# Performance work log

Measured on AMD Instinct MI355X. Metric: run time of the kernel, lower is better.

The kernel has to match this reference:

```python
import jax, jax.numpy as jnp
import numpy as np

N = 100000   # nodes
E = 1250000  # directed edges
K = 20000    # selected nodes
D_IN, D_H, D_OUT = 128, 64, 5
NEG_SLOPE = 0.01  # F.leaky_relu default
EPS = 1e-5        # BatchNorm eps


def setup_inputs() -> dict:
    key = jax.random.key(0)
    ks = jax.random.split(key, 13)
    x = jax.random.normal(ks[0], (N, D_IN), jnp.float32)
    edge_index = jax.random.randint(ks[1], (2, E), 0, N, dtype=jnp.int32)
    idx = jax.random.randint(ks[2], (K,), 0, N, dtype=jnp.int32)
    # GCNConv 0: glorot-style weights + zero bias
    W0 = jax.random.normal(ks[3], (D_IN, D_H), jnp.float32) * (1.0 / np.sqrt(D_IN))
    b0 = jnp.zeros((D_H,), jnp.float32)
    gamma0 = jnp.ones((D_H,), jnp.float32)
    beta0 = jnp.zeros((D_H,), jnp.float32)
    # GCNConv 1
    W1 = jax.random.normal(ks[4], (D_H, D_H), jnp.float32) * (1.0 / np.sqrt(D_H))
    b1 = jnp.zeros((D_H,), jnp.float32)
    gamma1 = jnp.ones((D_H,), jnp.float32)
    beta1 = jnp.zeros((D_H,), jnp.float32)
    # final MLP
    Wm = jax.random.normal(ks[5], (D_H, D_OUT), jnp.float32) * (1.0 / np.sqrt(D_H))
    bm = jnp.zeros((D_OUT,), jnp.float32)
    return {"x": x, "edge_index": edge_index, "idx": idx,
            "W0": W0, "b0": b0, "gamma0": gamma0, "beta0": beta0,
            "W1": W1, "b1": b1, "gamma1": gamma1, "beta1": beta1,
            "Wm": Wm, "bm": bm}


def reference(x, edge_index, idx, W0, b0, gamma0, beta0, W1, b1, gamma1, beta1, Wm, bm):
    n = x.shape[0]
    # GCNConv: add self-loops, symmetric normalization D^-1/2 A D^-1/2
    loops = jnp.arange(n, dtype=edge_index.dtype)
    row = jnp.concatenate([edge_index[0], loops])  # source
    col = jnp.concatenate([edge_index[1], loops])  # target
    deg = jax.ops.segment_sum(jnp.ones_like(col, dtype=x.dtype), col, num_segments=n)
    dis = jnp.where(deg > 0, jax.lax.rsqrt(jnp.maximum(deg, 1e-12)), 0.0)
    norm = dis[row] * dis[col]  # [E+N]

    def gcn_conv(h, W, b):
        hw = h @ W                                  # [N, d_out]
        msg = hw[row] * norm[:, None]               # gather + scale
        return jax.ops.segment_sum(msg, col, num_segments=n) + b  # scatter-add

    def batch_norm(h, g, b):  # training-mode BN over node dim
        mu = h.mean(axis=0)
        var = h.var(axis=0)
        return (h - mu) * jax.lax.rsqrt(var + EPS) * g + b

    h = jax.nn.leaky_relu(gcn_conv(x, W0, b0), NEG_SLOPE)
    h = batch_norm(h, gamma0, beta0)
    h = jax.nn.leaky_relu(gcn_conv(h, W1, b1), NEG_SLOPE)
    h = batch_norm(h, gamma1, beta1)
    h_sel = h[idx]                                   # index_select over nodes
    out = jax.nn.sigmoid(h_sel @ Wm + bm)
    return (h_sel, out)
```

## Files before the change

### kernel.cpp

```cpp
#include <hip/hip_runtime.h>

static constexpr float NEG_SLOPE = 0.01f;
static constexpr float BN_EPS = 1e-5f;

using f16 = _Float16;
using f16x4 = __attribute__((ext_vector_type(4))) _Float16;
using f32x4 = __attribute__((ext_vector_type(4))) float;

__global__ __launch_bounds__(256) void sentinel_kernel(float* out, int m, float val) {
  int i = blockIdx.x * 256 + threadIdx.x;
  if (i < m) out[i] = val;
}

__global__ __launch_bounds__(256) void zero_kernel(int* __restrict__ deg,
                                                   float* __restrict__ stats, int n) {
  int stride = gridDim.x * blockDim.x;
  for (int i = blockIdx.x * blockDim.x + threadIdx.x; i < n; i += stride) deg[i] = 0;
  if (blockIdx.x == 0 && threadIdx.x < 256) stats[threadIdx.x] = 0.f;
}

__global__ __launch_bounds__(256) void deg_kernel(const int* __restrict__ col,
                                                  int* __restrict__ deg, int E) {
  int t = blockIdx.x * 256 + threadIdx.x;
  int S = gridDim.x * 256;
  int e0 = t, e1 = t + S, e2 = t + 2 * S, e3 = t + 3 * S;
  int v0 = (e0 < E) ? col[e0] : -1;
  int v1 = (e1 < E) ? col[e1] : -1;
  int v2 = (e2 < E) ? col[e2] : -1;
  int v3 = (e3 < E) ? col[e3] : -1;
  if (v0 >= 0) atomicAdd(&deg[v0], 1);
  if (v1 >= 0) atomicAdd(&deg[v1], 1);
  if (v2 >= 0) atomicAdd(&deg[v2], 1);
  if (v3 >= 0) atomicAdd(&deg[v3], 1);
}

__global__ __launch_bounds__(256) void scan_partial(const int* __restrict__ deg,
                                                    int* __restrict__ partial, int n) {
  int i = blockIdx.x * 256 + threadIdx.x;
  int v = (i < n) ? deg[i] : 0;
  __shared__ int s[256];
  s[threadIdx.x] = v;
  __syncthreads();
  for (int off = 128; off; off >>= 1) {
    if (threadIdx.x < off) s[threadIdx.x] += s[threadIdx.x + off];
    __syncthreads();
  }
  if (threadIdx.x == 0) partial[blockIdx.x] = s[0];
}

__global__ __launch_bounds__(256) void scan_top(int* partial, int nb) {
  __shared__ int s[256];
  __shared__ int carry_s;
  if (threadIdx.x == 0) carry_s = 0;
  __syncthreads();
  for (int base = 0; base < nb; base += 256) {
    int i = base + threadIdx.x;
    int v = (i < nb) ? partial[i] : 0;
    s[threadIdx.x] = v;
    __syncthreads();
    for (int off = 1; off < 256; off <<= 1) {
      int t = (threadIdx.x >= off) ? s[threadIdx.x - off] : 0;
      __syncthreads();
      s[threadIdx.x] += t;
      __syncthreads();
    }
    int inc = s[threadIdx.x];
    int tot = s[255];
    int carry = carry_s;
    if (i < nb) partial[i] = carry + inc - v;
    __syncthreads();
    if (threadIdx.x == 0) carry_s = carry + tot;
    __syncthreads();
  }
}

__global__ __launch_bounds__(256) void scan_final(const int* __restrict__ deg,
                                                  const int* __restrict__ partial,
                                                  int* __restrict__ start,
                                                  int* __restrict__ cursor,
                                                  float* __restrict__ dis, int n, int E) {
  int i = blockIdx.x * 256 + threadIdx.x;
  int v = (i < n) ? deg[i] : 0;
  __shared__ int s[256];
  s[threadIdx.x] = v;
  __syncthreads();
  for (int off = 1; off < 256; off <<= 1) {
    int t = (threadIdx.x >= off) ? s[threadIdx.x - off] : 0;
    __syncthreads();
    s[threadIdx.x] += t;
    __syncthreads();
  }
  if (i < n) {
    int incl = partial[blockIdx.x] + s[threadIdx.x];
    start[i] = incl - v;
    cursor[i] = incl;
    dis[i] = rsqrtf((float)(v + 1));
  }
  if (i == 0) start[n] = E;
}

__global__ __launch_bounds__(256) void fill_kernel(
    const int* __restrict__ row, const int* __restrict__ colv,
    int* __restrict__ cursor, int* __restrict__ csr, int E) {
  int t = blockIdx.x * 256 + threadIdx.x;
  int S = gridDim.x * 256;
  int e0 = t, e1 = t + S, e2 = t + 2 * S, e3 = t + 3 * S;
  bool b0 = e0 < E, b1 = e1 < E, b2 = e2 < E, b3 = e3 < E;
  int v0 = 0, v1 = 0, v2 = 0, v3 = 0, r0 = 0, r1 = 0, r2 = 0, r3 = 0;
  if (b0) { v0 = colv[e0]; r0 = row[e0]; }
  if (b1) { v1 = colv[e1]; r1 = row[e1]; }
  if (b2) { v2 = colv[e2]; r2 = row[e2]; }
  if (b3) { v3 = colv[e3]; r3 = row[e3]; }
  int o0 = 0, o1 = 0, o2 = 0, o3 = 0;
  if (b0) o0 = atomicSub(&cursor[v0], 1) - 1;
  if (b1) o1 = atomicSub(&cursor[v1], 1) - 1;
  if (b2) o2 = atomicSub(&cursor[v2], 1) - 1;
  if (b3) o3 = atomicSub(&cursor[v3], 1) - 1;
  if (b0) csr[o0] = r0;
  if (b1) csr[o1] = r1;
  if (b2) csr[o2] = r2;
  if (b3) csr[o3] = r3;
}

template <int KD, bool FOLD, bool A_HALF>
__global__ __launch_bounds__(256) void mfma_gemm(
    const void* __restrict__ Aptr, const float* __restrict__ W,
    const float* __restrict__ sc, const float* __restrict__ cadd,
    const float* __restrict__ dis, f16* __restrict__ g, int n) {
  constexpr int NKT = KD / 16;
  const int lane = threadIdx.x & 63;
  const int wq = threadIdx.x >> 6;
  const int lr = lane & 15;
  const int kb = (lane >> 4) * 4;

  f16x4 bfrag[NKT][4];
#pragma unroll
  for (int kt = 0; kt < NKT; ++kt)
#pragma unroll
    for (int ct = 0; ct < 4; ++ct) {
#pragma unroll
      for (int j = 0; j < 4; ++j) {
        int k = kt * 16 + kb + j;
        float w = W[k * 64 + ct * 16 + lr];
        if (FOLD) w *= sc[k];
        bfrag[kt][ct][j] = (f16)w;
      }
    }
  float cl[4];
#pragma unroll
  for (int ct = 0; ct < 4; ++ct) cl[ct] = FOLD ? cadd[ct * 16 + lr] : 0.f;

  const int ntiles = (n + 15) >> 4;
  for (int t = blockIdx.x * 4 + wq; t < ntiles; t += gridDim.x * 4) {
    const int r0 = t << 4;
    int arow = r0 + lr;
    if (arow >= n) arow = n - 1;
    f16x4 afrag[NKT];
    if (A_HALF) {
      const f16* Ah = (const f16*)Aptr;
#pragma unroll
      for (int kt = 0; kt < NKT; ++kt)
        afrag[kt] = *reinterpret_cast<const f16x4*>(Ah + (size_t)arow * KD + kt * 16 + kb);
    } else {
      const float* Af = (const float*)Aptr;
#pragma unroll
      for (int kt = 0; kt < NKT; ++kt) {
        f32x4 xa = *reinterpret_cast<const f32x4*>(Af + (size_t)arow * KD + kt * 16 + kb);
        f16x4 a;
        a[0] = (f16)xa[0]; a[1] = (f16)xa[1]; a[2] = (f16)xa[2]; a[3] = (f16)xa[3];
        afrag[kt] = a;
      }
    }
    f32x4 acc[4];
#pragma unroll
    for (int ct = 0; ct < 4; ++ct) acc[ct] = (f32x4){0.f, 0.f, 0.f, 0.f};
#pragma unroll
    for (int kt = 0; kt < NKT; ++kt)
#pragma unroll
      for (int ct = 0; ct < 4; ++ct)
        acc[ct] = __builtin_amdgcn_mfma_f32_16x16x16f16(afrag[kt], bfrag[kt][ct], acc[ct], 0, 0, 0);
    if (r0 + 16 <= n) {
#pragma unroll
      for (int v = 0; v < 4; ++v) {
        int grow = r0 + (lane >> 4) * 4 + v;
        float dv = dis[grow];
#pragma unroll
        for (int ct = 0; ct < 4; ++ct)
          g[(size_t)grow * 64 + ct * 16 + lr] = (f16)((acc[ct][v] + cl[ct]) * dv);
      }
    } else {
      for (int v = 0; v < 4; ++v) {
        int grow = r0 + (lane >> 4) * 4 + v;
        if (grow < n) {
          float dv = dis[grow];
          for (int ct = 0; ct < 4; ++ct)
            g[(size_t)grow * 64 + ct * 16 + lr] = (f16)((acc[ct][v] + cl[ct]) * dv);
        }
      }
    }
  }
}

template <typename OutT>
__global__ __launch_bounds__(256) void gather_post(
    const f16* __restrict__ g, const int* __restrict__ csr,
    const int* __restrict__ start, const float* __restrict__ dis,
    const float* __restrict__ bias, OutT* __restrict__ t_out,
    float* __restrict__ stats, int n) {
  const int lane = threadIdx.x & 63;
  const float bd = bias[lane];
  const f16* gl = g + lane;
  const int wid = (blockIdx.x * 256 + threadIdx.x) >> 6;
  const int nw = (gridDim.x * 256) >> 6;
  float lsum = 0.f, lsq = 0.f;
  for (int v0 = wid * 2; v0 < n; v0 += nw * 2) {
    const int v1 = v0 + 1;
    const bool hasB = (v1 < n);
    int2 sv = *reinterpret_cast<const int2*>(start + v0);
    const int s0a = sv.x, s1a = sv.y;
    const int s0b = s1a;
    const int s1b = hasB ? start[v0 + 2] : s1a;
    float suma = (float)gl[v0 * 64];
    float sumb = hasB ? (float)gl[v1 * 64] : 0.f;
    int ea = s0a, eb = s0b;
    int nbat_a = (s1a - s0a + 15) >> 4;
    int nbat_b = (s1b - s0b + 15) >> 4;
    int nbatch = nbat_a > nbat_b ? nbat_a : nbat_b;
    for (int b = 0; b < nbatch; ++b) {
      int ua[16], ub[16];
#pragma unroll
      for (int i = 0; i < 16; ++i) ua[i] = (ea + i < s1a) ? csr[ea + i] : v0;
#pragma unroll
      for (int i = 0; i < 16; ++i) ub[i] = (eb + i < s1b) ? csr[eb + i] : v0;
      float fa[16], fb[16];
#pragma unroll
      for (int i = 0; i < 16; ++i) fa[i] = (float)gl[ua[i] * 64];
#pragma unroll
      for (int i = 0; i < 16; ++i) fb[i] = (float)gl[ub[i] * 64];
      float pa = 0.f, pb = 0.f;
#pragma unroll
      for (int i = 0; i < 16; ++i) pa += (ea + i < s1a) ? fa[i] : 0.f;
#pragma unroll
      for (int i = 0; i < 16; ++i) pb += (eb + i < s1b) ? fb[i] : 0.f;
      suma += pa;
      sumb += pb;
      ea += 16;
      eb += 16;
    }
    float ta = dis[v0] * suma + bd;
    ta = (ta > 0.f) ? ta : NEG_SLOPE * ta;
    t_out[(size_t)v0 * 64 + lane] = (OutT)ta;
    lsum += ta;
    lsq += ta * ta;
    if (hasB) {
      float tb = dis[v1] * sumb + bd;
      tb = (tb > 0.f) ? tb : NEG_SLOPE * tb;
      t_out[(size_t)v1 * 64 + lane] = (OutT)tb;
      lsum += tb;
      lsq += tb * tb;
    }
  }
  __shared__ float red[256];
  red[threadIdx.x] = lsum;
  __syncthreads();
  if (threadIdx.x < 64)
    atomicAdd(&stats[lane],
              red[threadIdx.x] + red[threadIdx.x + 64] + red[threadIdx.x + 128] + red[threadIdx.x + 192]);
  __syncthreads();
  red[threadIdx.x] = lsq;
  __syncthreads();
  if (threadIdx.x < 64)
    atomicAdd(&stats[64 + lane],
              red[threadIdx.x] + red[threadIdx.x + 64] + red[threadIdx.x + 128] + red[threadIdx.x + 192]);
}

__global__ __launch_bounds__(64) void bnparam_kernel(
    const float* __restrict__ stats, const float* __restrict__ gamma,
    const float* __restrict__ beta, const float* __restrict__ W,
    float* __restrict__ outp, int n, int withC) {
  int d = threadIdx.x;
  __shared__ float ssh[64];
  float inv_n = 1.0f / (float)n;
  float mu = stats[d] * inv_n;
  float var = stats[64 + d] * inv_n - mu * mu;
  float r = rsqrtf(var + BN_EPS);
  float s = gamma[d] * r;
  float sh = beta[d] - mu * s;
  outp[d] = s;
  outp[64 + d] = sh;
  ssh[d] = sh;
  __syncthreads();
  if (withC) {
    float c = 0.f;
    for (int k = 0; k < 64; ++k) c = fmaf(ssh[k], W[k * 64 + d], c);
    outp[128 + d] = c;
  }
}

__global__ __launch_bounds__(256) void selmlp_kernel(
    const float* __restrict__ t, const int* __restrict__ idx,
    const float* __restrict__ bnp, const float* __restrict__ Wm,
    const float* __restrict__ bm, float* __restrict__ out,
    float* __restrict__ out2, int K) {
  const int lane = threadIdx.x & 63;
  int w = (blockIdx.x * 256 + threadIdx.x) >> 6;
  if (w >= K) return;
  int v = idx[w];
  float hv = fmaf(t[(size_t)v * 64 + lane], bnp[lane], bnp[64 + lane]);
  out[(size_t)w * 64 + lane] = hv;
#pragma unroll
  for (int j = 0; j < 5; ++j) {
    float p = hv * Wm[lane * 5 + j];
#pragma unroll
    for (int off = 32; off; off >>= 1) p += __shfl_xor(p, off);
    if (lane == 0) out2[(size_t)w * 5 + j] = 1.f / (1.f + expf(-(p + bm[j])));
  }
}

extern "C" void kernel_launch(void* const* d_in, const int* in_sizes, int n_in,
                              void* d_out, int out_size, void* d_ws, size_t ws_size,
                              hipStream_t stream) {
  const float* x      = (const float*)d_in[0];
  const int*   eidx   = (const int*)d_in[1];
  const int*   idx    = (const int*)d_in[2];
  const float* W0     = (const float*)d_in[3];
  const float* b0     = (const float*)d_in[4];
  const float* gamma0 = (const float*)d_in[5];
  const float* beta0  = (const float*)d_in[6];
  const float* W1     = (const float*)d_in[7];
  const float* b1     = (const float*)d_in[8];
  const float* gamma1 = (const float*)d_in[9];
  const float* beta1  = (const float*)d_in[10];
  const float* Wm     = (const float*)d_in[11];
  const float* bm     = (const float*)d_in[12];

  const int n = in_sizes[0] / 128;
  const int E = in_sizes[1] / 2;
  const int K = in_sizes[2];
  const int* erow = eidx;
  const int* ecol = eidx + E;
  const int nb = (n + 255) / 256;

  size_t needed = (size_t)n * 64 * 4
                + 256 * 4 + 320 * 4
                + (size_t)n * 4
                + (size_t)n * 4
                + (size_t)(n + 1) * 4
                + (size_t)n * 4
                + (size_t)(E + 16) * 4
                + (size_t)(nb + 1) * 4
                + (size_t)n * 64 * 2
                + (size_t)n * 64 * 2;
  if (ws_size < needed) {
    sentinel_kernel<<<dim3((out_size + 255) / 256), dim3(256), 0, stream>>>(
        (float*)d_out, out_size, 1e6f);
    return;
  }
  float* tf    = (float*)d_ws;
  float* stats = tf + (size_t)n * 64;
  float* bnp   = stats + 256;
  float* dis   = bnp + 320;
  int*   deg   = (int*)(dis + n);
  int*   start = deg + n;
  int*   cursor = start + (n + 1);
  int*   csr   = cursor + n;
  int*   partial = csr + (E + 16);
  f16*   gh    = (f16*)(partial + nb + 1);
  f16*   t0h   = gh + (size_t)n * 64;

  dim3 blk(256);
  const int eb4 = (E + 1023) / 1024;
  zero_kernel<<<dim3(nb), blk, 0, stream>>>(deg, stats, n);
  deg_kernel<<<dim3(eb4), blk, 0, stream>>>(ecol, deg, E);
  scan_partial<<<dim3(nb), blk, 0, stream>>>(deg, partial, n);
  scan_top<<<dim3(1), blk, 0, stream>>>(partial, nb);
  scan_final<<<dim3(nb), blk, 0, stream>>>(deg, partial, start, cursor, dis, n, E);
  fill_kernel<<<dim3(eb4), blk, 0, stream>>>(erow, ecol, cursor, csr, E);

  mfma_gemm<128, false, false><<<dim3(640), blk, 0, stream>>>(
      x, W0, nullptr, nullptr, dis, gh, n);
  gather_post<f16><<<dim3(2048), blk, 0, stream>>>(gh, csr, start, dis, b0, t0h, stats, n);
  bnparam_kernel<<<dim3(1), dim3(64), 0, stream>>>(stats, gamma0, beta0, W1, bnp, n, 1);
  mfma_gemm<64, true, true><<<dim3(640), blk, 0, stream>>>(
      t0h, W1, bnp, bnp + 128, dis, gh, n);
  gather_post<float><<<dim3(2048), blk, 0, stream>>>(gh, csr, start, dis, b1, tf, stats + 128, n);
  bnparam_kernel<<<dim3(1), dim3(64), 0, stream>>>(
      stats + 128, gamma1, beta1, nullptr, bnp + 192, n, 0);
  selmlp_kernel<<<dim3((K + 3) / 4), blk, 0, stream>>>(
      tf, idx, bnp + 192, Wm, bm, (float*)d_out, (float*)d_out + (size_t)K * 64, K);
}
```

Before: 371.3 us.

## Pad CSR rows to 16 with a zero sentinel node and gather f16x2 per lane

Each node's CSR segment is padded to a multiple of 16 and filled with index n, which points at an extra zeroed row of the feature buffer. The gather loop can then use unconditional int4 index loads and sum without masks. The gather is also reorganised so each half-wave handles one node with 32 lanes loading f16x2 pairs, and the block reduction is done with float4 values. The cost is a larger CSR array plus extra sentinel loads for the padding slots, which amount to roughly 8 extra entries per node on average.

```diff
diff --git a/kernel.cpp b/kernel.cpp
--- a/kernel.cpp
+++ b/kernel.cpp
@@ -4,6 +4,7 @@
 static constexpr float BN_EPS = 1e-5f;
 
 using f16 = _Float16;
+using f16x2 = __attribute__((ext_vector_type(2))) _Float16;
 using f16x4 = __attribute__((ext_vector_type(4))) _Float16;
 using f32x4 = __attribute__((ext_vector_type(4))) float;
 
@@ -13,10 +14,12 @@
 }
 
 __global__ __launch_bounds__(256) void zero_kernel(int* __restrict__ deg,
-                                                   float* __restrict__ stats, int n) {
+                                                   float* __restrict__ stats,
+                                                   unsigned int* __restrict__ gzero, int n) {
   int stride = gridDim.x * blockDim.x;
   for (int i = blockIdx.x * blockDim.x + threadIdx.x; i < n; i += stride) deg[i] = 0;
   if (blockIdx.x == 0 && threadIdx.x < 256) stats[threadIdx.x] = 0.f;
+  if (blockIdx.x == 0 && threadIdx.x < 32) gzero[threadIdx.x] = 0u;
 }
 
 __global__ __launch_bounds__(256) void deg_kernel(const int* __restrict__ col,
@@ -37,9 +40,10 @@
 __global__ __launch_bounds__(256) void scan_partial(const int* __restrict__ deg,
                                                     int* __restrict__ partial, int n) {
   int i = blockIdx.x * 256 + threadIdx.x;
-  int v = (i < n) ? deg[i] : 0;
+  int d = (i < n) ? deg[i] : 0;
+  int pd = (d + 15) & ~15;
   __shared__ int s[256];
-  s[threadIdx.x] = v;
+  s[threadIdx.x] = pd;
   __syncthreads();
   for (int off = 128; off; off >>= 1) {
     if (threadIdx.x < off) s[threadIdx.x] += s[threadIdx.x + off];
@@ -76,13 +80,15 @@
 
 __global__ __launch_bounds__(256) void scan_final(const int* __restrict__ deg,
                                                   const int* __restrict__ partial,
-                                                  int* __restrict__ start,
+                                                  int* __restrict__ pstart,
                                                   int* __restrict__ cursor,
-                                                  float* __restrict__ dis, int n, int E) {
+                                                  int* __restrict__ csr,
+                                                  float* __restrict__ dis, int n) {
   int i = blockIdx.x * 256 + threadIdx.x;
-  int v = (i < n) ? deg[i] : 0;
+  int d = (i < n) ? deg[i] : 0;
+  int pd = (d + 15) & ~15;
   __shared__ int s[256];
-  s[threadIdx.x] = v;
+  s[threadIdx.x] = pd;
   __syncthreads();
   for (int off = 1; off < 256; off <<= 1) {
     int t = (threadIdx.x >= off) ? s[threadIdx.x - off] : 0;
@@ -92,11 +98,13 @@
   }
   if (i < n) {
     int incl = partial[blockIdx.x] + s[threadIdx.x];
-    start[i] = incl - v;
-    cursor[i] = incl;
-    dis[i] = rsqrtf((float)(v + 1));
-  }
-  if (i == 0) start[n] = E;
+    int ps = incl - pd;
+    pstart[i] = ps;
+    cursor[i] = ps + d;
+    dis[i] = rsqrtf((float)(d + 1));
+    for (int j = d; j < pd; ++j) csr[ps + j] = n;
+    if (i == n - 1) pstart[n] = incl;
+  }
 }
 
 __global__ __launch_bounds__(256) void fill_kernel(
@@ -201,77 +209,78 @@
   }
 }
 
-template <typename OutT>
-__global__ __launch_bounds__(256) void gather_post(
+template <int HOUT>
+__global__ __launch_bounds__(256) void gather_post2(
     const f16* __restrict__ g, const int* __restrict__ csr,
-    const int* __restrict__ start, const float* __restrict__ dis,
-    const float* __restrict__ bias, OutT* __restrict__ t_out,
+    const int* __restrict__ pstart, const float* __restrict__ dis,
+    const float* __restrict__ bias, void* __restrict__ t_out,
     float* __restrict__ stats, int n) {
-  const int lane = threadIdx.x & 63;
-  const float bd = bias[lane];
-  const f16* gl = g + lane;
-  const int wid = (blockIdx.x * 256 + threadIdx.x) >> 6;
+  const int tid = threadIdx.x;
+  const int fl = tid & 31;
+  const int half = (tid >> 5) & 1;
+  const float2 bd = reinterpret_cast<const float2*>(bias)[fl];
+  const f16x2* __restrict__ g2 = reinterpret_cast<const f16x2*>(g);
+  const int wid = (blockIdx.x * 256 + tid) >> 6;
   const int nw = (gridDim.x * 256) >> 6;
-  float lsum = 0.f, lsq = 0.f;
-  for (int v0 = wid * 2; v0 < n; v0 += nw * 2) {
-    const int v1 = v0 + 1;
-    const bool hasB = (v1 < n);
-    int2 sv = *reinterpret_cast<const int2*>(start + v0);
-    const int s0a = sv.x, s1a = sv.y;
-    const int s0b = s1a;
-    const int s1b = hasB ? start[v0 + 2] : s1a;
-    float suma = (float)gl[v0 * 64];
-    float sumb = hasB ? (float)gl[v1 * 64] : 0.f;
-    int ea = s0a, eb = s0b;
-    int nbat_a = (s1a - s0a + 15) >> 4;
-    int nbat_b = (s1b - s0b + 15) >> 4;
-    int nbatch = nbat_a > nbat_b ? nbat_a : nbat_b;
-    for (int b = 0; b < nbatch; ++b) {
-      int ua[16], ub[16];
-#pragma unroll
-      for (int i = 0; i < 16; ++i) ua[i] = (ea + i < s1a) ? csr[ea + i] : v0;
-#pragma unroll
-      for (int i = 0; i < 16; ++i) ub[i] = (eb + i < s1b) ? csr[eb + i] : v0;
-      float fa[16], fb[16];
-#pragma unroll
-      for (int i = 0; i < 16; ++i) fa[i] = (float)gl[ua[i] * 64];
-#pragma unroll
-      for (int i = 0; i < 16; ++i) fb[i] = (float)gl[ub[i] * 64];
-      float pa = 0.f, pb = 0.f;
-#pragma unroll
-      for (int i = 0; i < 16; ++i) pa += (ea + i < s1a) ? fa[i] : 0.f;
-#pragma unroll
-      for (int i = 0; i < 16; ++i) pb += (eb + i < s1b) ? fb[i] : 0.f;
-      suma += pa;
-      sumb += pb;
-      ea += 16;
-      eb += 16;
-    }
-    float ta = dis[v0] * suma + bd;
-    ta = (ta > 0.f) ? ta : NEG_SLOPE * ta;
-    t_out[(size_t)v0 * 64 + lane] = (OutT)ta;
-    lsum += ta;
-    lsq += ta * ta;
-    if (hasB) {
-      float tb = dis[v1] * sumb + bd;
-      tb = (tb > 0.f) ? tb : NEG_SLOPE * tb;
-      t_out[(size_t)v1 * 64 + lane] = (OutT)tb;
-      lsum += tb;
-      lsq += tb * tb;
-    }
-  }
-  __shared__ float red[256];
-  red[threadIdx.x] = lsum;
-  __syncthreads();
-  if (threadIdx.x < 64)
-    atomicAdd(&stats[lane],
-              red[threadIdx.x] + red[threadIdx.x + 64] + red[threadIdx.x + 128] + red[threadIdx.x + 192]);
-  __syncthreads();
-  red[threadIdx.x] = lsq;
-  __syncthreads();
-  if (threadIdx.x < 64)
-    atomicAdd(&stats[64 + lane],
-              red[threadIdx.x] + red[threadIdx.x + 64] + red[threadIdx.x + 128] + red[threadIdx.x + 192]);
+  float sx = 0.f, sy = 0.f, qx = 0.f, qy = 0.f;
+  for (int v = wid * 2 + half; v < n; v += nw * 2) {
+    const int ps = pstart[v];
+    const int pe = pstart[v + 1];
+    f16x2 sv = g2[v * 32 + fl];
+    float ax = (float)sv[0], ay = (float)sv[1];
+    for (int e = ps; e < pe; e += 16) {
+      const int4* c4 = reinterpret_cast<const int4*>(csr + e);
+      int4 ua = c4[0], ub = c4[1], uc = c4[2], ud = c4[3];
+      f16x2 d0 = g2[ua.x * 32 + fl], d1 = g2[ua.y * 32 + fl];
+      f16x2 d2 = g2[ua.z * 32 + fl], d3 = g2[ua.w * 32 + fl];
+      f16x2 d4 = g2[ub.x * 32 + fl], d5 = g2[ub.y * 32 + fl];
+      f16x2 d6 = g2[ub.z * 32 + fl], d7 = g2[ub.w * 32 + fl];
+      f16x2 d8 = g2[uc.x * 32 + fl], d9 = g2[uc.y * 32 + fl];
+      f16x2 da = g2[uc.z * 32 + fl], db = g2[uc.w * 32 + fl];
+      f16x2 dc = g2[ud.x * 32 + fl], dd = g2[ud.y * 32 + fl];
+      f16x2 de = g2[ud.z * 32 + fl], df = g2[ud.w * 32 + fl];
+      float px = (((float)d0[0] + (float)d1[0]) + ((float)d2[0] + (float)d3[0])) +
+                 (((float)d4[0] + (float)d5[0]) + ((float)d6[0] + (float)d7[0])) +
+                 (((float)d8[0] + (float)d9[0]) + ((float)da[0] + (float)db[0])) +
+                 (((float)dc[0] + (float)dd[0]) + ((float)de[0] + (float)df[0]));
+      float py = (((float)d0[1] + (float)d1[1]) + ((float)d2[1] + (float)d3[1])) +
+                 (((float)d4[1] + (float)d5[1]) + ((float)d6[1] + (float)d7[1])) +
+                 (((float)d8[1] + (float)d9[1]) + ((float)da[1] + (float)db[1])) +
+                 (((float)dc[1] + (float)dd[1]) + ((float)de[1] + (float)df[1]));
+      ax += px;
+      ay += py;
+    }
+    float dv = dis[v];
+    float tx = dv * ax + bd.x;
+    tx = (tx > 0.f) ? tx : NEG_SLOPE * tx;
+    float ty = dv * ay + bd.y;
+    ty = (ty > 0.f) ? ty : NEG_SLOPE * ty;
+    if (HOUT) {
+      f16x2 o;
+      o[0] = (f16)tx;
+      o[1] = (f16)ty;
+      reinterpret_cast<f16x2*>(t_out)[v * 32 + fl] = o;
+    } else {
+      reinterpret_cast<float2*>(t_out)[v * 32 + fl] = make_float2(tx, ty);
+    }
+    sx += tx; sy += ty;
+    qx += tx * tx; qy += ty * ty;
+  }
+  __shared__ float4 red[256];
+  red[tid] = make_float4(sx, sy, qx, qy);
+  __syncthreads();
+  if (tid < 32) {
+    float4 a = red[tid];
+#pragma unroll
+    for (int o = 32; o < 256; o += 32) {
+      float4 b = red[tid + o];
+      a.x += b.x; a.y += b.y; a.z += b.z; a.w += b.w;
+    }
+    atomicAdd(&stats[2 * tid], a.x);
+    atomicAdd(&stats[2 * tid + 1], a.y);
+    atomicAdd(&stats[64 + 2 * tid], a.z);
+    atomicAdd(&stats[64 + 2 * tid + 1], a.w);
+  }
 }
 
 __global__ __launch_bounds__(64) void bnparam_kernel(
@@ -340,50 +349,49 @@
   const int* erow = eidx;
   const int* ecol = eidx + E;
   const int nb = (n + 255) / 256;
+  const size_t Ecap = (size_t)E + 16 * (size_t)n;
 
   size_t needed = (size_t)n * 64 * 4
+                + ((size_t)n + 1) * 64 * 2
+                + (size_t)n * 64 * 2
+                + (size_t)n * 4 * 3
+                + ((size_t)n + 4) * 4
+                + Ecap * 4
                 + 256 * 4 + 320 * 4
-                + (size_t)n * 4
-                + (size_t)n * 4
-                + (size_t)(n + 1) * 4
-                + (size_t)n * 4
-                + (size_t)(E + 16) * 4
-                + (size_t)(nb + 1) * 4
-                + (size_t)n * 64 * 2
-                + (size_t)n * 64 * 2;
+                + (size_t)(nb + 4) * 4;
   if (ws_size < needed) {
     sentinel_kernel<<<dim3((out_size + 255) / 256), dim3(256), 0, stream>>>(
         (float*)d_out, out_size, 1e6f);
     return;
   }
-  float* tf    = (float*)d_ws;
-  float* stats = tf + (size_t)n * 64;
-  float* bnp   = stats + 256;
-  float* dis   = bnp + 320;
-  int*   deg   = (int*)(dis + n);
-  int*   start = deg + n;
-  int*   cursor = start + (n + 1);
-  int*   csr   = cursor + n;
-  int*   partial = csr + (E + 16);
-  f16*   gh    = (f16*)(partial + nb + 1);
-  f16*   t0h   = gh + (size_t)n * 64;
+  float* tf     = (float*)d_ws;
+  f16*   gh     = (f16*)(tf + (size_t)n * 64);
+  f16*   t0h    = gh + ((size_t)n + 1) * 64;
+  float* dis    = (float*)(t0h + (size_t)n * 64);
+  int*   deg    = (int*)(dis + n);
+  int*   pstart = deg + n;
+  int*   cursor = pstart + (n + 4);
+  int*   csr    = cursor + n;
+  float* stats  = (float*)(csr + Ecap);
+  float* bnp    = stats + 256;
+  int*   partial = (int*)(bnp + 320);
 
   dim3 blk(256);
   const int eb4 = (E + 1023) / 1024;
-  zero_kernel<<<dim3(nb), blk, 0, stream>>>(deg, stats, n);
+  zero_kernel<<<dim3(nb), blk, 0, stream>>>(deg, stats, (unsigned int*)(gh + (size_t)n * 64), n);
   deg_kernel<<<dim3(eb4), blk, 0, stream>>>(ecol, deg, E);
   scan_partial<<<dim3(nb), blk, 0, stream>>>(deg, partial, n);
   scan_top<<<dim3(1), blk, 0, stream>>>(partial, nb);
-  scan_final<<<dim3(nb), blk, 0, stream>>>(deg, partial, start, cursor, dis, n, E);
+  scan_final<<<dim3(nb), blk, 0, stream>>>(deg, partial, pstart, cursor, csr, dis, n);
   fill_kernel<<<dim3(eb4), blk, 0, stream>>>(erow, ecol, cursor, csr, E);
 
   mfma_gemm<128, false, false><<<dim3(640), blk, 0, stream>>>(
       x, W0, nullptr, nullptr, dis, gh, n);
-  gather_post<f16><<<dim3(2048), blk, 0, stream>>>(gh, csr, start, dis, b0, t0h, stats, n);
+  gather_post2<1><<<dim3(2048), blk, 0, stream>>>(gh, csr, pstart, dis, b0, t0h, stats, n);
   bnparam_kernel<<<dim3(1), dim3(64), 0, stream>>>(stats, gamma0, beta0, W1, bnp, n, 1);
   mfma_gemm<64, true, true><<<dim3(640), blk, 0, stream>>>(
       t0h, W1, bnp, bnp + 128, dis, gh, n);
-  gather_post<float><<<dim3(2048), blk, 0, stream>>>(gh, csr, start, dis, b1, tf, stats + 128, n);
+  gather_post2<0><<<dim3(2048), blk, 0, stream>>>(gh, csr, pstart, dis, b1, tf, stats + 128, n);
   bnparam_kernel<<<dim3(1), dim3(64), 0, stream>>>(
       stats + 128, gamma1, beta1, nullptr, bnp + 192, n, 0);
   selmlp_kernel<<<dim3((K + 3) / 4), blk, 0, stream>>>(
```

Measured after the change: 490.7 us. 1.32x slower.
